# Performance work log

Hardware: AMD Instinct MI355X
Metric: run time of the kernel (lower is better)

## Reference

```python
import jax, jax.numpy as jnp
import numpy as np

B, N, D, H, K, FFN = 8, 256, 512, 16, 4, 2048
DK = D // H
NEG = -1e12


def _lin(k, i, o):
    return jax.random.normal(k, (i, o), jnp.float32) / np.sqrt(i)


def setup_inputs() -> dict:
    key = jax.random.key(0)
    ks = jax.random.split(key, 12)
    return {
        "x": jax.random.normal(ks[0], (B, N, D), jnp.float32),
        "dist": jax.random.uniform(ks[1], (B, N - 1, N - 1), jnp.float32) * 10.0,
        "dist_bar": jnp.array([1.5, 3.0, 5.0, 8.0], jnp.float32),
        "attn_bias": 0.1 * jax.random.normal(ks[2], (B, K, N, N), jnp.float32),
        "mask": jnp.ones((B, 1, N, N), jnp.int32),
        "num_heads": H,
        "Wq": _lin(ks[3], D, D), "bq": jnp.zeros((D,), jnp.float32),
        "Wk": _lin(ks[4], D, D), "bk": jnp.zeros((D,), jnp.float32),
        "Wv": _lin(ks[5], D, D), "bv": jnp.zeros((D,), jnp.float32),
        "W1": _lin(ks[6], K * D, D), "b1": jnp.zeros((D,), jnp.float32),
        "W2": _lin(ks[7], D, D), "b2": jnp.zeros((D,), jnp.float32),
        "g1": jnp.ones((D,), jnp.float32), "be1": jnp.zeros((D,), jnp.float32),
        "Wf1": _lin(ks[8], D, FFN), "bf1": jnp.zeros((FFN,), jnp.float32),
        "Wf2": _lin(ks[9], FFN, D), "bf2": jnp.zeros((D,), jnp.float32),
        "g2": jnp.ones((D,), jnp.float32), "be2": jnp.zeros((D,), jnp.float32),
    }


def _ln(x, g, b, eps=1e-6):
    m = jnp.mean(x, -1, keepdims=True)
    v = jnp.mean((x - m) ** 2, -1, keepdims=True)
    return (x - m) / jnp.sqrt(v + eps) * g + b


def _forward(x, dist, dist_bar, attn_bias, mask, num_heads,
             Wq, bq, Wk, bk, Wv, bv, W1, b1, W2, b2, g1, be1,
             Wf1, bf1, Wf2, bf2, g2, be2):
    Bn, Nn, Dn = x.shape
    Hh = num_heads
    dk = Dn // Hh
    Kk = dist_bar.shape[0]

    q = (x @ Wq + bq).reshape(Bn, Nn, Hh, dk).transpose(0, 2, 1, 3)  # [B,H,N,dk]
    k = (x @ Wk + bk).reshape(Bn, Nn, Hh, dk).transpose(0, 2, 1, 3)
    v = (x @ Wv + bv).reshape(Bn, Nn, Hh, dk).transpose(0, 2, 1, 3)

    scores = jnp.einsum('bhnd,bhmd->bhnm', q, k) / np.sqrt(dk)      # [B,H,N,N]
    # expand over scales and add bias: [B,H,K,N,N]
    scores = scores[:, :, None, :, :] + attn_bias[:, None, :, :, :]
    # padding mask [B,1,N,N] -> broadcast over H,K
    scores = jnp.where(mask[:, None] == 0, NEG, scores)

    # build padded distance with super node (row/col 0 distance = 0)
    nd = jnp.ones((Bn, Nn, Nn), x.dtype)
    nd = nd.at[:, 1:, 1:].set(dist)
    nd = nd.at[:, 0, :].set(0.0).at[:, :, 0].set(0.0)
    masks = nd[:, None, None, :, :] < dist_bar.reshape(1, 1, Kk, 1, 1)  # [B,1,K,N,N]
    masks = masks.at[:, :, :, 0, :].set(True).at[:, :, :, :, 0].set(True)

    scores = jnp.where(masks, scores, NEG)
    attn = jax.nn.softmax(scores, axis=-1)                           # [B,H,K,N,N]

    msg = jnp.einsum('bhknm,bhmd->bhknd', attn, v)                   # [B,H,K,N,dk]
    # faithful to torch: transpose(1,2).view(B,H*K,N,dk) then transpose(2,3).view(B,N,-1)
    msg = jnp.transpose(msg, (0, 2, 1, 3, 4)).reshape(Bn, Kk * Hh, Nn, dk)
    msg = jnp.transpose(msg, (0, 1, 3, 2)).reshape(Bn, Nn, Kk * Hh * dk)

    h = jax.nn.silu(msg @ W1 + b1) @ W2 + b2
    y = _ln(h + x, g1, be1)

    f = jax.nn.gelu(y @ Wf1 + bf1, approximate=False) @ Wf2 + bf2
    out = _ln(f + y, g2, be2)
    return out


def reference(x, dist, dist_bar, attn_bias, mask, num_heads,
              Wq, bq, Wk, bk, Wv, bv, W1, b1, W2, b2, g1, be1,
              Wf1, bf1, Wf2, bf2, g2, be2):
    return _forward(x, dist, dist_bar, attn_bias, mask, num_heads,
                    Wq, bq, Wk, bk, Wv, bv, W1, b1, W2, b2, g1, be1,
                    Wf1, bf1, Wf2, bf2, g2, be2)
```

## Files before the change

kernel.cpp:

```cpp
#include <hip/hip_runtime.h>
#include <math.h>

#define BB 8
#define NN 256
#define DD 512
#define HH 16
#define KK 4
#define DKK 32
#define FFN_ 2048
#define NEGV -1e12f

typedef __attribute__((ext_vector_type(8))) short bf16x8;
typedef __attribute__((ext_vector_type(4))) float f32x4;

__device__ __forceinline__ unsigned short f2bf(float f) {
    union { float f; unsigned int u; } v; v.f = f;
    unsigned int r = (v.u + 0x7FFFu + ((v.u >> 16) & 1u)) >> 16;
    return (unsigned short)r;
}
__device__ __forceinline__ float bf2f(unsigned short u) {
    union { unsigned int i; float f; } v; v.i = ((unsigned int)u) << 16;
    return v.f;
}
__device__ __forceinline__ void gload_lds16(const unsigned short* g, unsigned short* l) {
    __builtin_amdgcn_global_load_lds(
        (const __attribute__((address_space(1))) void*)g,
        (__attribute__((address_space(3))) void*)l, 16, 0, 0);
}

__global__ __launch_bounds__(256) void prep_kernel(
    const float* __restrict__ x,
    const float* __restrict__ Wq, const float* __restrict__ Wk,
    const float* __restrict__ Wv, const float* __restrict__ W1,
    const float* __restrict__ W2, const float* __restrict__ Wf1,
    const float* __restrict__ Wf2,
    const float* __restrict__ bq, const float* __restrict__ bk,
    const float* __restrict__ bv,
    unsigned short* __restrict__ xb, unsigned short* __restrict__ Wqkvt,
    unsigned short* __restrict__ W1t, unsigned short* __restrict__ W2t,
    unsigned short* __restrict__ Wf1t, unsigned short* __restrict__ Wf2t,
    float* __restrict__ bqkv)
{
    const int z = blockIdx.z;
    const int t = threadIdx.x;

    if (z == 7) {
        const int i0 = blockIdx.x * 1024 + t * 4;
        float4 xv = *(const float4*)(x + i0);
        ushort4 o;
        o.x = f2bf(xv.x); o.y = f2bf(xv.y); o.z = f2bf(xv.z); o.w = f2bf(xv.w);
        *(ushort4*)(xb + i0) = o;
        return;
    }
    if (z == 8) {
        if (blockIdx.x >= 6) return;
        const int i = blockIdx.x * 256 + t;
        float v = (i < 512) ? bq[i] : (i < 1024) ? bk[i - 512] : bv[i - 1024];
        bqkv[i] = v;
        return;
    }

    const float* src; unsigned short* dst; int Kd, Nd;
    switch (z) {
        case 0: src = Wq;  dst = Wqkvt;              Kd = 512;  Nd = 512;  break;
        case 1: src = Wk;  dst = Wqkvt + 512 * 512;  Kd = 512;  Nd = 512;  break;
        case 2: src = Wv;  dst = Wqkvt + 1024 * 512; Kd = 512;  Nd = 512;  break;
        case 3: src = W1;  dst = W1t;  Kd = 2048; Nd = 512;  break;
        case 4: src = W2;  dst = W2t;  Kd = 512;  Nd = 512;  break;
        case 5: src = Wf1; dst = Wf1t; Kd = 512;  Nd = 2048; break;
        default: src = Wf2; dst = Wf2t; Kd = 2048; Nd = 512; break;
    }
    const int ktiles = Kd / 32, ntiles = Nd / 32;
    const int ti = blockIdx.x;
    if (ti >= ktiles * ntiles) return;
    const int k0 = (ti % ktiles) * 32, n0 = (ti / ktiles) * 32;

    __shared__ float tile[32][33];
    const int xx = t & 31, yy = t >> 5;
    #pragma unroll
    for (int r = 0; r < 4; ++r)
        tile[yy * 4 + r][xx] = src[(size_t)(k0 + yy * 4 + r) * Nd + n0 + xx];
    __syncthreads();
    #pragma unroll
    for (int r = 0; r < 4; ++r)
        dst[(size_t)(n0 + yy * 4 + r) * Kd + k0 + xx] = f2bf(tile[xx][yy * 4 + r]);
}

__global__ __launch_bounds__(256) void prep_bias(
    const float* __restrict__ attn_bias, const int* __restrict__ mask,
    const float* __restrict__ dist, const float* __restrict__ dist_bar,
    unsigned short* __restrict__ biasMs)
{
    const int bx = blockIdx.x;
    const int rg = bx & 63, ks = (bx >> 6) & 3, b = bx >> 8;
    const int m = threadIdx.x;
    const float bar = dist_bar[ks];

    ushort4 o;
    unsigned short* po = (unsigned short*)&o;
    #pragma unroll
    for (int i = 0; i < 4; ++i) {
        const int n = rg * 4 + i;
        const int mk = mask[((size_t)(b * NN) + n) * NN + m];
        bool allowed = (n == 0) || (m == 0);
        if (!allowed)
            allowed = dist[((size_t)(b * 255) + (n - 1)) * 255 + (m - 1)] < bar;
        const float bias = attn_bias[(((size_t)(b * KK) + ks) * NN + n) * NN + m];
        po[i] = f2bf((mk != 0 && allowed) ? bias : NEGV);
    }
    *(ushort4*)(biasMs + (size_t)bx * 1024 + m * 4) = o;
}

template<int ACT, int EPI>
__global__ __launch_bounds__(256) void mfma_gemm128(
    const unsigned short* __restrict__ A, const unsigned short* __restrict__ Bt,
    const float* __restrict__ bias, unsigned short* __restrict__ Cb,
    unsigned short* __restrict__ vT, int M, int N, int Kdim)
{
    __shared__ unsigned short As[128 * 64];
    __shared__ unsigned short Bs[128 * 64];

    const int t = threadIdx.x, lane = t & 63, wv = t >> 6;
    const int n0 = blockIdx.x * 128, m0 = blockIdx.y * 128;
    const int wm = wv >> 1, wn = wv & 1;
    const int L = lane & 15, qd = lane >> 4;
    const int sr = lane >> 3, sc = lane & 7;

    f32x4 acc[4][4];
    #pragma unroll
    for (int i = 0; i < 4; ++i)
        #pragma unroll
        for (int j = 0; j < 4; ++j) acc[i][j] = (f32x4){0.f, 0.f, 0.f, 0.f};

    for (int kt = 0; kt < Kdim; kt += 64) {
        #pragma unroll
        for (int p = 0; p < 4; ++p) {
            const int rbase = wv * 32 + p * 8;
            gload_lds16(A  + (size_t)(m0 + rbase + sr) * Kdim + kt + sc * 8,
                        As + rbase * 64);
            gload_lds16(Bt + (size_t)(n0 + rbase + sr) * Kdim + kt + sc * 8,
                        Bs + rbase * 64);
        }
        __syncthreads();
        #pragma unroll
        for (int s = 0; s < 2; ++s) {
            bf16x8 af[4], bf[4];
            #pragma unroll
            for (int i = 0; i < 4; ++i)
                af[i] = *(const bf16x8*)(As + (wm * 64 + i * 16 + L) * 64 + s * 32 + qd * 8);
            #pragma unroll
            for (int j = 0; j < 4; ++j)
                bf[j] = *(const bf16x8*)(Bs + (wn * 64 + j * 16 + L) * 64 + s * 32 + qd * 8);
            #pragma unroll
            for (int i = 0; i < 4; ++i)
                #pragma unroll
                for (int j = 0; j < 4; ++j)
                    acc[i][j] = __builtin_amdgcn_mfma_f32_16x16x32_bf16(af[i], bf[j], acc[i][j], 0, 0, 0);
        }
        __syncthreads();
    }

    #pragma unroll
    for (int j = 0; j < 4; ++j) {
        const int col = n0 + wn * 64 + j * 16 + L;
        const float bv = bias[col];
        #pragma unroll
        for (int i = 0; i < 4; ++i) {
            const int rowb = m0 + wm * 64 + i * 16 + qd * 4;
            if (EPI == 1 && col >= 1024) {
                ushort4 pk;
                unsigned short* pp = (unsigned short*)&pk;
                #pragma unroll
                for (int r = 0; r < 4; ++r) pp[r] = f2bf(acc[i][j][r] + bv);
                *(ushort4*)(vT + (size_t)(col - 1024) * 2048 + rowb) = pk;
            } else {
                #pragma unroll
                for (int r = 0; r < 4; ++r) {
                    float v = acc[i][j][r] + bv;
                    if (ACT == 1) v = v / (1.0f + __expf(-v));
                    else if (ACT == 2) v = 0.5f * v * (1.0f + erff(v * 0.70710678118654752f));
                    Cb[(size_t)(rowb + r) * N + col] = f2bf(v);
                }
            }
        }
    }
}

template<int ACT>
__global__ __launch_bounds__(256) void mfma_gemm64(
    const unsigned short* __restrict__ A, const unsigned short* __restrict__ Bt,
    const float* __restrict__ bias, unsigned short* __restrict__ Cb,
    int M, int N, int Kdim)
{
    __shared__ unsigned short As[64 * 64];
    __shared__ unsigned short Bs[64 * 64];

    const int t = threadIdx.x, lane = t & 63, wv = t >> 6;
    const int n0 = blockIdx.x * 64, m0 = blockIdx.y * 64;
    const int r8 = lane >> 3, c8 = lane & 7;
    const int L = lane & 15, qd = lane >> 4;

    f32x4 acc[4];
    #pragma unroll
    for (int j = 0; j < 4; ++j) acc[j] = (f32x4){0.f, 0.f, 0.f, 0.f};

    for (int kt = 0; kt < Kdim; kt += 64) {
        #pragma unroll
        for (int i = 0; i < 2; ++i) {
            const int rbase = wv * 16 + i * 8;
            gload_lds16(A  + (size_t)(m0 + rbase + r8) * Kdim + kt + c8 * 8, As + rbase * 64);
            gload_lds16(Bt + (size_t)(n0 + rbase + r8) * Kdim + kt + c8 * 8, Bs + rbase * 64);
        }
        __syncthreads();
        #pragma unroll
        for (int s = 0; s < 2; ++s) {
            const bf16x8 a = *(const bf16x8*)(As + (wv * 16 + L) * 64 + s * 32 + qd * 8);
            #pragma unroll
            for (int j = 0; j < 4; ++j) {
                const bf16x8 b = *(const bf16x8*)(Bs + (j * 16 + L) * 64 + s * 32 + qd * 8);
                acc[j] = __builtin_amdgcn_mfma_f32_16x16x32_bf16(a, b, acc[j], 0, 0, 0);
            }
        }
        __syncthreads();
    }

    #pragma unroll
    for (int j = 0; j < 4; ++j) {
        const int col = n0 + j * 16 + L;
        const float bv = bias[col];
        #pragma unroll
        for (int r = 0; r < 4; ++r) {
            const int row = m0 + wv * 16 + qd * 4 + r;
            float v = acc[j][r] + bv;
            if (ACT == 1) v = v / (1.0f + __expf(-v));
            else if (ACT == 2) v = 0.5f * v * (1.0f + erff(v * 0.70710678118654752f));
            Cb[(size_t)row * N + col] = f2bf(v);
        }
    }
}

__global__ __launch_bounds__(256) void attn_kernel(
    const unsigned short* __restrict__ qkvb, const unsigned short* __restrict__ vT,
    const unsigned short* __restrict__ biasMs, unsigned short* __restrict__ msgT)
{
    const int qt = blockIdx.x, h = blockIdx.y, b = blockIdx.z;
    const int q0 = qt * 64;
    const int t = threadIdx.x, lane = t & 63, wv = t >> 6;
    const int L = lane & 15, qd = lane >> 4;

    __shared__ unsigned short Qs[64 * 32];
    __shared__ unsigned short Ks[256 * 32];
    __shared__ unsigned short Vs[32 * 264];
    __shared__ unsigned short Ps[64 * 264];
    __shared__ unsigned short Ot[32 * 72];

    {
        const int r = lane >> 2, c = lane & 3;
        gload_lds16(qkvb + (size_t)(b * NN + q0 + wv * 16 + r) * 1536 + h * DKK + c * 8,
                    Qs + wv * 16 * 32);
        #pragma unroll
        for (int p = 0; p < 4; ++p)
            gload_lds16(qkvb + (size_t)(b * NN + p * 64 + wv * 16 + r) * 1536 + 512 + h * DKK + c * 8,
                        Ks + (p * 64 + wv * 16) * 32);
    }
    {
        const int vr = t >> 3, seg = t & 7;
        const unsigned short* gv = vT + (size_t)(h * DKK + vr) * 2048 + b * NN + seg * 32;
        #pragma unroll
        for (int i = 0; i < 4; ++i) {
            bf16x8 vv = *(const bf16x8*)(gv + i * 8);
            *(bf16x8*)(Vs + vr * 264 + seg * 32 + i * 8) = vv;
        }
    }
    __syncthreads();

    f32x4 S[16];
    #pragma unroll
    for (int j = 0; j < 16; ++j) S[j] = (f32x4){0.f, 0.f, 0.f, 0.f};
    {
        const bf16x8 aq = *(const bf16x8*)(Qs + (wv * 16 + L) * 32 + qd * 8);
        #pragma unroll
        for (int j = 0; j < 16; ++j) {
            const bf16x8 bk = *(const bf16x8*)(Ks + (j * 16 + L) * 32 + qd * 8);
            S[j] = __builtin_amdgcn_mfma_f32_16x16x32_bf16(aq, bk, S[j], 0, 0, 0);
        }
    }
    const float scale = 0.17677669529663687f;
    const int rgb = (q0 + wv * 16) >> 2;

    for (int ks = 0; ks < KK; ++ks) {
        const unsigned short* bp = biasMs + ((size_t)((b * KK + ks) * 64 + rgb + qd)) * 1024;

        ushort4 b4[16];
        float mx[4] = {-3e38f, -3e38f, -3e38f, -3e38f};
        #pragma unroll
        for (int j = 0; j < 16; ++j) {
            b4[j] = *(const ushort4*)(bp + (j * 16 + L) * 4);
            const unsigned short* pb = (const unsigned short*)&b4[j];
            #pragma unroll
            for (int r = 0; r < 4; ++r)
                mx[r] = fmaxf(mx[r], S[j][r] * scale + bf2f(pb[r]));
        }
        #pragma unroll
        for (int off = 8; off > 0; off >>= 1)
            #pragma unroll
            for (int r = 0; r < 4; ++r)
                mx[r] = fmaxf(mx[r], __shfl_xor(mx[r], off));

        float sm[4] = {0.f, 0.f, 0.f, 0.f};
        #pragma unroll
        for (int j = 0; j < 16; ++j) {
            const unsigned short* pb = (const unsigned short*)&b4[j];
            #pragma unroll
            for (int r = 0; r < 4; ++r) {
                const float e = __expf(S[j][r] * scale + bf2f(pb[r]) - mx[r]);
                sm[r] += e;
                Ps[(wv * 16 + qd * 4 + r) * 264 + j * 16 + L] = f2bf(e);
            }
        }
        #pragma unroll
        for (int off = 8; off > 0; off >>= 1)
            #pragma unroll
            for (int r = 0; r < 4; ++r)
                sm[r] += __shfl_xor(sm[r], off);
        float inv[4];
        #pragma unroll
        for (int r = 0; r < 4; ++r) inv[r] = 1.0f / sm[r];

        f32x4 O[2];
        O[0] = (f32x4){0.f, 0.f, 0.f, 0.f};
        O[1] = (f32x4){0.f, 0.f, 0.f, 0.f};
        #pragma unroll
        for (int kc = 0; kc < 8; ++kc) {
            const bf16x8 ap = *(const bf16x8*)(Ps + (wv * 16 + L) * 264 + kc * 32 + qd * 8);
            #pragma unroll
            for (int jt = 0; jt < 2; ++jt) {
                const bf16x8 bv = *(const bf16x8*)(Vs + (jt * 16 + L) * 264 + kc * 32 + qd * 8);
                O[jt] = __builtin_amdgcn_mfma_f32_16x16x32_bf16(ap, bv, O[jt], 0, 0, 0);
            }
        }
        #pragma unroll
        for (int jt = 0; jt < 2; ++jt)
            #pragma unroll
            for (int r = 0; r < 4; ++r)
                Ot[(jt * 16 + L) * 72 + wv * 16 + qd * 4 + r] = f2bf(O[jt][r] * inv[r]);
        __syncthreads();

        {
            const int dd = t >> 3, cc = t & 7;
            bf16x8 ov = *(const bf16x8*)(Ot + dd * 72 + cc * 8);
            *(bf16x8*)(msgT + (size_t)b * 524288 +
                       ((size_t)((ks * HH + h) * DKK + dd)) * NN + q0 + cc * 8) = ov;
        }
        __syncthreads();
    }
}

__global__ __launch_bounds__(256) void ln_kernel(
    const unsigned short* __restrict__ a, const float* __restrict__ r,
    const float* __restrict__ g, const float* __restrict__ be,
    float* __restrict__ out, unsigned short* __restrict__ outb)
{
    const int row = blockIdx.x;
    const int t = threadIdx.x;
    __shared__ float red[256];

    const size_t base = (size_t)row * DD;
    const float z0 = bf2f(a[base + t]) + r[base + t];
    const float z1 = bf2f(a[base + 256 + t]) + r[base + 256 + t];

    red[t] = z0 + z1; __syncthreads();
    for (int s = 128; s > 0; s >>= 1) {
        if (t < s) red[t] += red[t + s];
        __syncthreads();
    }
    const float mean = red[0] * (1.0f / 512.0f); __syncthreads();

    const float d0 = z0 - mean, d1 = z1 - mean;
    red[t] = d0 * d0 + d1 * d1; __syncthreads();
    for (int s = 128; s > 0; s >>= 1) {
        if (t < s) red[t] += red[t + s];
        __syncthreads();
    }
    const float inv = rsqrtf(red[0] * (1.0f / 512.0f) + 1e-6f);

    const float o0 = d0 * inv * g[t] + be[t];
    const float o1 = d1 * inv * g[256 + t] + be[256 + t];
    out[base + t] = o0;
    out[base + 256 + t] = o1;
    if (outb) {
        outb[base + t] = f2bf(o0);
        outb[base + 256 + t] = f2bf(o1);
    }
}

extern "C" void kernel_launch(void* const* d_in, const int* in_sizes, int n_in,
                              void* d_out, int out_size, void* d_ws, size_t ws_size,
                              hipStream_t stream)
{
    const float* x         = (const float*)d_in[0];
    const float* dist      = (const float*)d_in[1];
    const float* dist_bar  = (const float*)d_in[2];
    const float* attn_bias = (const float*)d_in[3];
    const int*   mask      = (const int*)d_in[4];
    const float* Wq  = (const float*)d_in[6];  const float* bq  = (const float*)d_in[7];
    const float* Wk  = (const float*)d_in[8];  const float* bk  = (const float*)d_in[9];
    const float* Wv  = (const float*)d_in[10]; const float* bv  = (const float*)d_in[11];
    const float* W1  = (const float*)d_in[12]; const float* b1  = (const float*)d_in[13];
    const float* W2  = (const float*)d_in[14]; const float* b2  = (const float*)d_in[15];
    const float* g1  = (const float*)d_in[16]; const float* be1 = (const float*)d_in[17];
    const float* Wf1 = (const float*)d_in[18]; const float* bf1 = (const float*)d_in[19];
    const float* Wf2 = (const float*)d_in[20]; const float* bf2 = (const float*)d_in[21];
    const float* g2  = (const float*)d_in[22]; const float* be2 = (const float*)d_in[23];

    float* ws = (float*)d_ws;
    unsigned short* qkvb   = (unsigned short*)(ws + 0);
    float*          yb     = ws + 0;
    unsigned short* vT     = (unsigned short*)(ws + 1572864);
    unsigned short* h1     = (unsigned short*)(ws + 1572864);
    unsigned short* xb     = (unsigned short*)(ws + 2097152);
    unsigned short* msgT   = (unsigned short*)(ws + 2097152);
    unsigned short* g3     = msgT;
    unsigned short* biasMs = (unsigned short*)(ws + 4194304);
    unsigned short* h2     = (unsigned short*)(ws + 4194304);
    unsigned short* fb     = h2;
    float*          bqkv   = ws + 5242880;
    unsigned short* yb16   = (unsigned short*)(ws + 5242880);
    unsigned short* Wqkvt  = (unsigned short*)(ws + 5767168);
    unsigned short* W1t    = (unsigned short*)(ws + 6160384);
    unsigned short* W2t    = (unsigned short*)(ws + 6684672);
    unsigned short* Wf1t   = (unsigned short*)(ws + 6815744);
    unsigned short* Wf2t   = (unsigned short*)(ws + 7340032);
    float*          outp   = (float*)d_out;

    dim3 thr(256);
    const int M = BB * NN;

    prep_kernel<<<dim3(1024, 1, 9), thr, 0, stream>>>(
        x, Wq, Wk, Wv, W1, W2, Wf1, Wf2, bq, bk, bv,
        xb, Wqkvt, W1t, W2t, Wf1t, Wf2t, bqkv);
    prep_bias<<<dim3(2048), thr, 0, stream>>>(attn_bias, mask, dist, dist_bar, biasMs);

    mfma_gemm128<0,1><<<dim3(12, 16), thr, 0, stream>>>(xb, Wqkvt, bqkv, qkvb, vT, M, 1536, DD);

    attn_kernel<<<dim3(4, HH, BB), thr, 0, stream>>>(qkvb, vT, biasMs, msgT);

    mfma_gemm64<1><<<dim3(8, 32), thr, 0, stream>>>(msgT, W1t, b1, h1, M, DD, 2048);
    mfma_gemm64<0><<<dim3(8, 32), thr, 0, stream>>>(h1, W2t, b2, h2, M, DD, DD);

    ln_kernel<<<dim3(M), thr, 0, stream>>>(h2, x, g1, be1, yb, yb16);

    mfma_gemm128<2,0><<<dim3(16, 16), thr, 0, stream>>>(yb16, Wf1t, bf1, g3, nullptr, M, FFN_, DD);
    mfma_gemm64<0><<<dim3(8, 32), thr, 0, stream>>>(g3, Wf2t, bf2, fb, M, DD, 2048);

    ln_kernel<<<dim3(M), thr, 0, stream>>>(fb, yb, g2, be2, outp, nullptr);
}
```

Baseline: 267.0 us.

## Use 512-thread 128x128 GEMMs with split-K partials and fused bias/LN finishers

Replaces the 128x128 and 64x64 GEMM kernels with one 512-thread, 8-wave 128x128 tile kernel. The narrow-N GEMMs (W1, W2, Wf2) use split-K into fp32 partial buffers, reduced by new finisher kernels that also apply bias plus SiLU, or bias, residual and LayerNorm. The bias/mask preparation is merged into the weight-prep kernel as an extra grid slice, which removes a launch, and the workspace layout is rearranged to hold the partials. The aim is more waves per CU and better GPU fill for the 2048x512 outputs. The cost is extra fp32 partial traffic and additional finisher passes.

```diff
diff --git a/kernel.cpp b/kernel.cpp
--- a/kernel.cpp
+++ b/kernel.cpp
@@ -36,15 +36,18 @@
     const float* __restrict__ Wf2,
     const float* __restrict__ bq, const float* __restrict__ bk,
     const float* __restrict__ bv,
+    const float* __restrict__ attn_bias, const int* __restrict__ mask,
+    const float* __restrict__ dist, const float* __restrict__ dist_bar,
     unsigned short* __restrict__ xb, unsigned short* __restrict__ Wqkvt,
     unsigned short* __restrict__ W1t, unsigned short* __restrict__ W2t,
     unsigned short* __restrict__ Wf1t, unsigned short* __restrict__ Wf2t,
-    float* __restrict__ bqkv)
+    float* __restrict__ bqkv, unsigned short* __restrict__ biasMs)
 {
     const int z = blockIdx.z;
     const int t = threadIdx.x;
 
     if (z == 7) {
+        if (blockIdx.x >= 1024) return;
         const int i0 = blockIdx.x * 1024 + t * 4;
         float4 xv = *(const float4*)(x + i0);
         ushort4 o;
@@ -57,6 +60,26 @@
         const int i = blockIdx.x * 256 + t;
         float v = (i < 512) ? bq[i] : (i < 1024) ? bk[i - 512] : bv[i - 1024];
         bqkv[i] = v;
+        return;
+    }
+    if (z == 9) {
+        const int bx = blockIdx.x;
+        const int rg = bx & 63, ks = (bx >> 6) & 3, b = bx >> 8;
+        const int m = t;
+        const float bar = dist_bar[ks];
+        ushort4 o;
+        unsigned short* po = (unsigned short*)&o;
+        #pragma unroll
+        for (int i = 0; i < 4; ++i) {
+            const int n = rg * 4 + i;
+            const int mk = mask[((size_t)(b * NN) + n) * NN + m];
+            bool allowed = (n == 0) || (m == 0);
+            if (!allowed)
+                allowed = dist[((size_t)(b * 255) + (n - 1)) * 255 + (m - 1)] < bar;
+            const float bias = attn_bias[(((size_t)(b * KK) + ks) * NN + n) * NN + m];
+            po[i] = f2bf((mk != 0 && allowed) ? bias : NEGV);
+        }
+        *(ushort4*)(biasMs + (size_t)bx * 1024 + m * 4) = o;
         return;
     }
 
@@ -86,36 +109,12 @@
         dst[(size_t)(n0 + yy * 4 + r) * Kd + k0 + xx] = f2bf(tile[xx][yy * 4 + r]);
 }
 
-__global__ __launch_bounds__(256) void prep_bias(
-    const float* __restrict__ attn_bias, const int* __restrict__ mask,
-    const float* __restrict__ dist, const float* __restrict__ dist_bar,
-    unsigned short* __restrict__ biasMs)
-{
-    const int bx = blockIdx.x;
-    const int rg = bx & 63, ks = (bx >> 6) & 3, b = bx >> 8;
-    const int m = threadIdx.x;
-    const float bar = dist_bar[ks];
-
-    ushort4 o;
-    unsigned short* po = (unsigned short*)&o;
-    #pragma unroll
-    for (int i = 0; i < 4; ++i) {
-        const int n = rg * 4 + i;
-        const int mk = mask[((size_t)(b * NN) + n) * NN + m];
-        bool allowed = (n == 0) || (m == 0);
-        if (!allowed)
-            allowed = dist[((size_t)(b * 255) + (n - 1)) * 255 + (m - 1)] < bar;
-        const float bias = attn_bias[(((size_t)(b * KK) + ks) * NN + n) * NN + m];
-        po[i] = f2bf((mk != 0 && allowed) ? bias : NEGV);
-    }
-    *(ushort4*)(biasMs + (size_t)bx * 1024 + m * 4) = o;
-}
-
-template<int ACT, int EPI>
-__global__ __launch_bounds__(256) void mfma_gemm128(
+template<int ACT, int EPI, int KSPLIT>
+__global__ __launch_bounds__(512) void mfma_gemm512(
     const unsigned short* __restrict__ A, const unsigned short* __restrict__ Bt,
     const float* __restrict__ bias, unsigned short* __restrict__ Cb,
-    unsigned short* __restrict__ vT, int M, int N, int Kdim)
+    unsigned short* __restrict__ vT, float* __restrict__ Cp,
+    int M, int N, int Kdim)
 {
     __shared__ unsigned short As[128 * 64];
     __shared__ unsigned short Bs[128 * 64];
@@ -126,16 +125,19 @@
     const int L = lane & 15, qd = lane >> 4;
     const int sr = lane >> 3, sc = lane & 7;
 
-    f32x4 acc[4][4];
-    #pragma unroll
-    for (int i = 0; i < 4; ++i)
+    const int ksub = Kdim / KSPLIT;
+    const int kbeg = blockIdx.z * ksub;
+
+    f32x4 acc[2][4];
+    #pragma unroll
+    for (int i = 0; i < 2; ++i)
         #pragma unroll
         for (int j = 0; j < 4; ++j) acc[i][j] = (f32x4){0.f, 0.f, 0.f, 0.f};
 
-    for (int kt = 0; kt < Kdim; kt += 64) {
-        #pragma unroll
-        for (int p = 0; p < 4; ++p) {
-            const int rbase = wv * 32 + p * 8;
+    for (int kt = kbeg; kt < kbeg + ksub; kt += 64) {
+        #pragma unroll
+        for (int p = 0; p < 2; ++p) {
+            const int rbase = wv * 16 + p * 8;
             gload_lds16(A  + (size_t)(m0 + rbase + sr) * Kdim + kt + sc * 8,
                         As + rbase * 64);
             gload_lds16(Bt + (size_t)(n0 + rbase + sr) * Kdim + kt + sc * 8,
@@ -144,18 +146,18 @@
         __syncthreads();
         #pragma unroll
         for (int s = 0; s < 2; ++s) {
-            bf16x8 af[4], bf[4];
-            #pragma unroll
-            for (int i = 0; i < 4; ++i)
-                af[i] = *(const bf16x8*)(As + (wm * 64 + i * 16 + L) * 64 + s * 32 + qd * 8);
+            bf16x8 af[2], bfb[4];
+            #pragma unroll
+            for (int i = 0; i < 2; ++i)
+                af[i] = *(const bf16x8*)(As + (wm * 32 + i * 16 + L) * 64 + s * 32 + qd * 8);
             #pragma unroll
             for (int j = 0; j < 4; ++j)
-                bf[j] = *(const bf16x8*)(Bs + (wn * 64 + j * 16 + L) * 64 + s * 32 + qd * 8);
-            #pragma unroll
-            for (int i = 0; i < 4; ++i)
+                bfb[j] = *(const bf16x8*)(Bs + (wn * 64 + j * 16 + L) * 64 + s * 32 + qd * 8);
+            #pragma unroll
+            for (int i = 0; i < 2; ++i)
                 #pragma unroll
                 for (int j = 0; j < 4; ++j)
-                    acc[i][j] = __builtin_amdgcn_mfma_f32_16x16x32_bf16(af[i], bf[j], acc[i][j], 0, 0, 0);
+                    acc[i][j] = __builtin_amdgcn_mfma_f32_16x16x32_bf16(af[i], bfb[j], acc[i][j], 0, 0, 0);
         }
         __syncthreads();
     }
@@ -163,17 +165,22 @@
     #pragma unroll
     for (int j = 0; j < 4; ++j) {
         const int col = n0 + wn * 64 + j * 16 + L;
-        const float bv = bias[col];
-        #pragma unroll
-        for (int i = 0; i < 4; ++i) {
-            const int rowb = m0 + wm * 64 + i * 16 + qd * 4;
-            if (EPI == 1 && col >= 1024) {
+        #pragma unroll
+        for (int i = 0; i < 2; ++i) {
+            const int rowb = m0 + wm * 32 + i * 16 + qd * 4;
+            if (EPI == 2) {
+                float* cp = Cp + (size_t)blockIdx.z * M * N + (size_t)rowb * N + col;
+                #pragma unroll
+                for (int r = 0; r < 4; ++r) cp[(size_t)r * N] = acc[i][j][r];
+            } else if (EPI == 1 && col >= 1024) {
+                const float bv = bias[col];
                 ushort4 pk;
                 unsigned short* pp = (unsigned short*)&pk;
                 #pragma unroll
                 for (int r = 0; r < 4; ++r) pp[r] = f2bf(acc[i][j][r] + bv);
                 *(ushort4*)(vT + (size_t)(col - 1024) * 2048 + rowb) = pk;
             } else {
+                const float bv = bias[col];
                 #pragma unroll
                 for (int r = 0; r < 4; ++r) {
                     float v = acc[i][j][r] + bv;
@@ -186,56 +193,70 @@
     }
 }
 
-template<int ACT>
-__global__ __launch_bounds__(256) void mfma_gemm64(
-    const unsigned short* __restrict__ A, const unsigned short* __restrict__ Bt,
-    const float* __restrict__ bias, unsigned short* __restrict__ Cb,
-    int M, int N, int Kdim)
-{
-    __shared__ unsigned short As[64 * 64];
-    __shared__ unsigned short Bs[64 * 64];
-
-    const int t = threadIdx.x, lane = t & 63, wv = t >> 6;
-    const int n0 = blockIdx.x * 64, m0 = blockIdx.y * 64;
-    const int r8 = lane >> 3, c8 = lane & 7;
-    const int L = lane & 15, qd = lane >> 4;
-
-    f32x4 acc[4];
-    #pragma unroll
-    for (int j = 0; j < 4; ++j) acc[j] = (f32x4){0.f, 0.f, 0.f, 0.f};
-
-    for (int kt = 0; kt < Kdim; kt += 64) {
-        #pragma unroll
-        for (int i = 0; i < 2; ++i) {
-            const int rbase = wv * 16 + i * 8;
-            gload_lds16(A  + (size_t)(m0 + rbase + r8) * Kdim + kt + c8 * 8, As + rbase * 64);
-            gload_lds16(Bt + (size_t)(n0 + rbase + r8) * Kdim + kt + c8 * 8, Bs + rbase * 64);
-        }
-        __syncthreads();
-        #pragma unroll
-        for (int s = 0; s < 2; ++s) {
-            const bf16x8 a = *(const bf16x8*)(As + (wv * 16 + L) * 64 + s * 32 + qd * 8);
-            #pragma unroll
-            for (int j = 0; j < 4; ++j) {
-                const bf16x8 b = *(const bf16x8*)(Bs + (j * 16 + L) * 64 + s * 32 + qd * 8);
-                acc[j] = __builtin_amdgcn_mfma_f32_16x16x32_bf16(a, b, acc[j], 0, 0, 0);
-            }
-        }
-        __syncthreads();
-    }
-
-    #pragma unroll
-    for (int j = 0; j < 4; ++j) {
-        const int col = n0 + j * 16 + L;
-        const float bv = bias[col];
-        #pragma unroll
-        for (int r = 0; r < 4; ++r) {
-            const int row = m0 + wv * 16 + qd * 4 + r;
-            float v = acc[j][r] + bv;
-            if (ACT == 1) v = v / (1.0f + __expf(-v));
-            else if (ACT == 2) v = 0.5f * v * (1.0f + erff(v * 0.70710678118654752f));
-            Cb[(size_t)row * N + col] = f2bf(v);
-        }
+__global__ __launch_bounds__(256) void fin_silu(
+    const float* __restrict__ Cp, const float* __restrict__ bias,
+    unsigned short* __restrict__ out)
+{
+    const int row = blockIdx.x, t = threadIdx.x;
+    const int c0 = t * 2;
+    const size_t base = (size_t)row * DD;
+    float sx = 0.f, sy = 0.f;
+    #pragma unroll
+    for (int z = 0; z < 4; ++z) {
+        const float2 p = *(const float2*)(Cp + (size_t)z * (2048u * 512u) + base + c0);
+        sx += p.x; sy += p.y;
+    }
+    float v0 = sx + bias[c0], v1 = sy + bias[c0 + 1];
+    v0 = v0 / (1.0f + __expf(-v0));
+    v1 = v1 / (1.0f + __expf(-v1));
+    ushort2 pk; pk.x = f2bf(v0); pk.y = f2bf(v1);
+    *(ushort2*)(out + base + c0) = pk;
+}
+
+template<int KS, int OUT16>
+__global__ __launch_bounds__(256) void fin_ln(
+    const float* __restrict__ Cp, const float* __restrict__ bias,
+    const float* __restrict__ res, const float* __restrict__ g,
+    const float* __restrict__ be, float* __restrict__ out,
+    unsigned short* __restrict__ outb)
+{
+    const int row = blockIdx.x, t = threadIdx.x;
+    const int c0 = t * 2;
+    const size_t base = (size_t)row * DD;
+    __shared__ float red[256];
+
+    float sx = 0.f, sy = 0.f;
+    #pragma unroll
+    for (int z = 0; z < KS; ++z) {
+        const float2 p = *(const float2*)(Cp + (size_t)z * (2048u * 512u) + base + c0);
+        sx += p.x; sy += p.y;
+    }
+    const float2 rv = *(const float2*)(res + base + c0);
+    const float z0 = sx + bias[c0]     + rv.x;
+    const float z1 = sy + bias[c0 + 1] + rv.y;
+
+    red[t] = z0 + z1; __syncthreads();
+    for (int s = 128; s > 0; s >>= 1) {
+        if (t < s) red[t] += red[t + s];
+        __syncthreads();
+    }
+    const float mean = red[0] * (1.0f / 512.0f); __syncthreads();
+
+    const float d0 = z0 - mean, d1 = z1 - mean;
+    red[t] = d0 * d0 + d1 * d1; __syncthreads();
+    for (int s = 128; s > 0; s >>= 1) {
+        if (t < s) red[t] += red[t + s];
+        __syncthreads();
+    }
+    const float inv = rsqrtf(red[0] * (1.0f / 512.0f) + 1e-6f);
+
+    const float o0 = d0 * inv * g[c0]     + be[c0];
+    const float o1 = d1 * inv * g[c0 + 1] + be[c0 + 1];
+    out[base + c0]     = o0;
+    out[base + c0 + 1] = o1;
+    if (OUT16) {
+        ushort2 pk; pk.x = f2bf(o0); pk.y = f2bf(o1);
+        *(ushort2*)(outb + base + c0) = pk;
     }
 }
 
@@ -353,44 +374,6 @@
                        ((size_t)((ks * HH + h) * DKK + dd)) * NN + q0 + cc * 8) = ov;
         }
         __syncthreads();
-    }
-}
-
-__global__ __launch_bounds__(256) void ln_kernel(
-    const unsigned short* __restrict__ a, const float* __restrict__ r,
-    const float* __restrict__ g, const float* __restrict__ be,
-    float* __restrict__ out, unsigned short* __restrict__ outb)
-{
-    const int row = blockIdx.x;
-    const int t = threadIdx.x;
-    __shared__ float red[256];
-
-    const size_t base = (size_t)row * DD;
-    const float z0 = bf2f(a[base + t]) + r[base + t];
-    const float z1 = bf2f(a[base + 256 + t]) + r[base + 256 + t];
-
-    red[t] = z0 + z1; __syncthreads();
-    for (int s = 128; s > 0; s >>= 1) {
-        if (t < s) red[t] += red[t + s];
-        __syncthreads();
-    }
-    const float mean = red[0] * (1.0f / 512.0f); __syncthreads();
-
-    const float d0 = z0 - mean, d1 = z1 - mean;
-    red[t] = d0 * d0 + d1 * d1; __syncthreads();
-    for (int s = 128; s > 0; s >>= 1) {
-        if (t < s) red[t] += red[t + s];
-        __syncthreads();
-    }
-    const float inv = rsqrtf(red[0] * (1.0f / 512.0f) + 1e-6f);
-
-    const float o0 = d0 * inv * g[t] + be[t];
-    const float o1 = d1 * inv * g[256 + t] + be[256 + t];
-    out[base + t] = o0;
-    out[base + 256 + t] = o1;
-    if (outb) {
-        outb[base + t] = f2bf(o0);
-        outb[base + 256 + t] = f2bf(o1);
     }
 }
 
@@ -415,43 +398,47 @@
 
     float* ws = (float*)d_ws;
     unsigned short* qkvb   = (unsigned short*)(ws + 0);
-    float*          yb     = ws + 0;
     unsigned short* vT     = (unsigned short*)(ws + 1572864);
-    unsigned short* h1     = (unsigned short*)(ws + 1572864);
     unsigned short* xb     = (unsigned short*)(ws + 2097152);
-    unsigned short* msgT   = (unsigned short*)(ws + 2097152);
+    unsigned short* msgT   = (unsigned short*)(ws + 2621440);
     unsigned short* g3     = msgT;
-    unsigned short* biasMs = (unsigned short*)(ws + 4194304);
-    unsigned short* h2     = (unsigned short*)(ws + 4194304);
-    unsigned short* fb     = h2;
-    float*          bqkv   = ws + 5242880;
-    unsigned short* yb16   = (unsigned short*)(ws + 5242880);
-    unsigned short* Wqkvt  = (unsigned short*)(ws + 5767168);
-    unsigned short* W1t    = (unsigned short*)(ws + 6160384);
-    unsigned short* W2t    = (unsigned short*)(ws + 6684672);
-    unsigned short* Wf1t   = (unsigned short*)(ws + 6815744);
-    unsigned short* Wf2t   = (unsigned short*)(ws + 7340032);
+    unsigned short* biasMs = (unsigned short*)(ws + 4718592);
+    float*          bqkv   = ws + 5767168;
+    unsigned short* h1     = (unsigned short*)(ws + 5771264);
+    float*          yb     = ws + 6295552;
+    unsigned short* yb16   = (unsigned short*)(ws + 7344128);
+    unsigned short* Wqkvt  = (unsigned short*)(ws + 7868416);
+    unsigned short* W1t    = (unsigned short*)(ws + 8261632);
+    unsigned short* W2t    = (unsigned short*)(ws + 8785920);
+    unsigned short* Wf1t   = (unsigned short*)(ws + 8916992);
+    unsigned short* Wf2t   = (unsigned short*)(ws + 9441280);
+    float*          part   = ws + 9965568;
     float*          outp   = (float*)d_out;
 
-    dim3 thr(256);
     const int M = BB * NN;
 
-    prep_kernel<<<dim3(1024, 1, 9), thr, 0, stream>>>(
+    prep_kernel<<<dim3(2048, 1, 10), dim3(256), 0, stream>>>(
         x, Wq, Wk, Wv, W1, W2, Wf1, Wf2, bq, bk, bv,
-        xb, Wqkvt, W1t, W2t, Wf1t, Wf2t, bqkv);
-    prep_bias<<<dim3(2048), thr, 0, stream>>>(attn_bias, mask, dist, dist_bar, biasMs);
-
-    mfma_gemm128<0,1><<<dim3(12, 16), thr, 0, stream>>>(xb, Wqkvt, bqkv, qkvb, vT, M, 1536, DD);
-
-    attn_kernel<<<dim3(4, HH, BB), thr, 0, stream>>>(qkvb, vT, biasMs, msgT);
-
-    mfma_gemm64<1><<<dim3(8, 32), thr, 0, stream>>>(msgT, W1t, b1, h1, M, DD, 2048);
-    mfma_gemm64<0><<<dim3(8, 32), thr, 0, stream>>>(h1, W2t, b2, h2, M, DD, DD);
-
-    ln_kernel<<<dim3(M), thr, 0, stream>>>(h2, x, g1, be1, yb, yb16);
-
-    mfma_gemm128<2,0><<<dim3(16, 16), thr, 0, stream>>>(yb16, Wf1t, bf1, g3, nullptr, M, FFN_, DD);
-    mfma_gemm64<0><<<dim3(8, 32), thr, 0, stream>>>(g3, Wf2t, bf2, fb, M, DD, 2048);
-
-    ln_kernel<<<dim3(M), thr, 0, stream>>>(fb, yb, g2, be2, outp, nullptr);
-}
+        attn_bias, mask, dist, dist_bar,
+        xb, Wqkvt, W1t, W2t, Wf1t, Wf2t, bqkv, biasMs);
+
+    mfma_gemm512<0,1,1><<<dim3(12, 16, 1), dim3(512), 0, stream>>>(
+        xb, Wqkvt, bqkv, qkvb, vT, nullptr, M, 1536, DD);
+
+    attn_kernel<<<dim3(4, HH, BB), dim3(256), 0, stream>>>(qkvb, vT, biasMs, msgT);
+
+    mfma_gemm512<0,2,4><<<dim3(4, 16, 4), dim3(512), 0, stream>>>(
+        msgT, W1t, nullptr, nullptr, nullptr, part, M, DD, 2048);
+    fin_silu<<<dim3(M), dim3(256), 0, stream>>>(part, b1, h1);
+
+    mfma_gemm512<0,2,2><<<dim3(4, 16, 2), dim3(512), 0, stream>>>(
+        h1, W2t, nullptr, nullptr, nullptr, part, M, DD, DD);
+    fin_ln<2,1><<<dim3(M), dim3(256), 0, stream>>>(part, b2, x, g1, be1, yb, yb16);
+
+    mfma_gemm512<2,0,1><<<dim3(16, 16, 1), dim3(512), 0, stream>>>(
+        yb16, Wf1t, bf1, g3, nullptr, nullptr, M, FFN_, DD);
+
+    mfma_gemm512<0,2,4><<<dim3(4, 16, 4), dim3(512), 0, stream>>>(
+        g3, Wf2t, nullptr, nullptr, nullptr, part, M, DD, 2048);
+    fin_ln<4,0><<<dim3(M), dim3(256), 0, stream>>>(part, bf2, yb, g2, be2, outp, nullptr);
+}
```

New measurement: 254.0 us. -4.9%, faster.

## Fuse output GEMMs with LayerNorm, fold bias prep, widen 128-tile GEMM to 512 threads

Applied to the files above, without the earlier changes.

The W2 and Wf2 projections are fused with the residual add and LayerNorm in a new gemm_ln kernel. Each of its blocks computes 16 full 512-wide rows, so the bf16 intermediate round trip and the separate LN launches go away. The attention bias/mask preparation is merged into prep_kernel as an extra grid slice. The 128x128 GEMM now runs with 8 waves of 512 threads, each computing a 32x64 sub-tile, to raise occupancy. The trade-off is that gemm_ln launches only 128 blocks, and every block reloads the whole 512-column weight slab each K step, which lowers parallelism for the K=2048 FFN down-projection.

```diff
diff --git a/kernel.cpp b/kernel.cpp
--- a/kernel.cpp
+++ b/kernel.cpp
@@ -36,15 +36,18 @@
     const float* __restrict__ Wf2,
     const float* __restrict__ bq, const float* __restrict__ bk,
     const float* __restrict__ bv,
+    const float* __restrict__ attn_bias, const int* __restrict__ mask,
+    const float* __restrict__ dist, const float* __restrict__ dist_bar,
     unsigned short* __restrict__ xb, unsigned short* __restrict__ Wqkvt,
     unsigned short* __restrict__ W1t, unsigned short* __restrict__ W2t,
     unsigned short* __restrict__ Wf1t, unsigned short* __restrict__ Wf2t,
-    float* __restrict__ bqkv)
+    float* __restrict__ bqkv, unsigned short* __restrict__ biasMs)
 {
     const int z = blockIdx.z;
     const int t = threadIdx.x;
 
     if (z == 7) {
+        if (blockIdx.x >= 1024) return;
         const int i0 = blockIdx.x * 1024 + t * 4;
         float4 xv = *(const float4*)(x + i0);
         ushort4 o;
@@ -57,6 +60,25 @@
         const int i = blockIdx.x * 256 + t;
         float v = (i < 512) ? bq[i] : (i < 1024) ? bk[i - 512] : bv[i - 1024];
         bqkv[i] = v;
+        return;
+    }
+    if (z == 9) {
+        const int bx = blockIdx.x;
+        const int rg = bx & 63, ks = (bx >> 6) & 3, b = bx >> 8;
+        const int m = t;
+        const float bar = dist_bar[ks];
+        ushort4 o; unsigned short* po = (unsigned short*)&o;
+        #pragma unroll
+        for (int i = 0; i < 4; ++i) {
+            const int n = rg * 4 + i;
+            const int mk = mask[((size_t)(b * NN) + n) * NN + m];
+            bool allowed = (n == 0) || (m == 0);
+            if (!allowed)
+                allowed = dist[((size_t)(b * 255) + (n - 1)) * 255 + (m - 1)] < bar;
+            const float bias = attn_bias[(((size_t)(b * KK) + ks) * NN + n) * NN + m];
+            po[i] = f2bf((mk != 0 && allowed) ? bias : NEGV);
+        }
+        *(ushort4*)(biasMs + (size_t)bx * 1024 + m * 4) = o;
         return;
     }
 
@@ -86,33 +108,8 @@
         dst[(size_t)(n0 + yy * 4 + r) * Kd + k0 + xx] = f2bf(tile[xx][yy * 4 + r]);
 }
 
-__global__ __launch_bounds__(256) void prep_bias(
-    const float* __restrict__ attn_bias, const int* __restrict__ mask,
-    const float* __restrict__ dist, const float* __restrict__ dist_bar,
-    unsigned short* __restrict__ biasMs)
-{
-    const int bx = blockIdx.x;
-    const int rg = bx & 63, ks = (bx >> 6) & 3, b = bx >> 8;
-    const int m = threadIdx.x;
-    const float bar = dist_bar[ks];
-
-    ushort4 o;
-    unsigned short* po = (unsigned short*)&o;
-    #pragma unroll
-    for (int i = 0; i < 4; ++i) {
-        const int n = rg * 4 + i;
-        const int mk = mask[((size_t)(b * NN) + n) * NN + m];
-        bool allowed = (n == 0) || (m == 0);
-        if (!allowed)
-            allowed = dist[((size_t)(b * 255) + (n - 1)) * 255 + (m - 1)] < bar;
-        const float bias = attn_bias[(((size_t)(b * KK) + ks) * NN + n) * NN + m];
-        po[i] = f2bf((mk != 0 && allowed) ? bias : NEGV);
-    }
-    *(ushort4*)(biasMs + (size_t)bx * 1024 + m * 4) = o;
-}
-
 template<int ACT, int EPI>
-__global__ __launch_bounds__(256) void mfma_gemm128(
+__global__ __launch_bounds__(512) void mfma_gemm512(
     const unsigned short* __restrict__ A, const unsigned short* __restrict__ Bt,
     const float* __restrict__ bias, unsigned short* __restrict__ Cb,
     unsigned short* __restrict__ vT, int M, int N, int Kdim)
@@ -126,16 +123,16 @@
     const int L = lane & 15, qd = lane >> 4;
     const int sr = lane >> 3, sc = lane & 7;
 
-    f32x4 acc[4][4];
-    #pragma unroll
-    for (int i = 0; i < 4; ++i)
+    f32x4 acc[2][4];
+    #pragma unroll
+    for (int i = 0; i < 2; ++i)
         #pragma unroll
         for (int j = 0; j < 4; ++j) acc[i][j] = (f32x4){0.f, 0.f, 0.f, 0.f};
 
     for (int kt = 0; kt < Kdim; kt += 64) {
         #pragma unroll
-        for (int p = 0; p < 4; ++p) {
-            const int rbase = wv * 32 + p * 8;
+        for (int p = 0; p < 2; ++p) {
+            const int rbase = wv * 16 + p * 8;
             gload_lds16(A  + (size_t)(m0 + rbase + sr) * Kdim + kt + sc * 8,
                         As + rbase * 64);
             gload_lds16(Bt + (size_t)(n0 + rbase + sr) * Kdim + kt + sc * 8,
@@ -144,18 +141,18 @@
         __syncthreads();
         #pragma unroll
         for (int s = 0; s < 2; ++s) {
-            bf16x8 af[4], bf[4];
-            #pragma unroll
-            for (int i = 0; i < 4; ++i)
-                af[i] = *(const bf16x8*)(As + (wm * 64 + i * 16 + L) * 64 + s * 32 + qd * 8);
+            bf16x8 af[2], bfb[4];
+            #pragma unroll
+            for (int i = 0; i < 2; ++i)
+                af[i] = *(const bf16x8*)(As + (wm * 32 + i * 16 + L) * 64 + s * 32 + qd * 8);
             #pragma unroll
             for (int j = 0; j < 4; ++j)
-                bf[j] = *(const bf16x8*)(Bs + (wn * 64 + j * 16 + L) * 64 + s * 32 + qd * 8);
-            #pragma unroll
-            for (int i = 0; i < 4; ++i)
+                bfb[j] = *(const bf16x8*)(Bs + (wn * 64 + j * 16 + L) * 64 + s * 32 + qd * 8);
+            #pragma unroll
+            for (int i = 0; i < 2; ++i)
                 #pragma unroll
                 for (int j = 0; j < 4; ++j)
-                    acc[i][j] = __builtin_amdgcn_mfma_f32_16x16x32_bf16(af[i], bf[j], acc[i][j], 0, 0, 0);
+                    acc[i][j] = __builtin_amdgcn_mfma_f32_16x16x32_bf16(af[i], bfb[j], acc[i][j], 0, 0, 0);
         }
         __syncthreads();
     }
@@ -165,11 +162,10 @@
         const int col = n0 + wn * 64 + j * 16 + L;
         const float bv = bias[col];
         #pragma unroll
-        for (int i = 0; i < 4; ++i) {
-            const int rowb = m0 + wm * 64 + i * 16 + qd * 4;
+        for (int i = 0; i < 2; ++i) {
+            const int rowb = m0 + wm * 32 + i * 16 + qd * 4;
             if (EPI == 1 && col >= 1024) {
-                ushort4 pk;
-                unsigned short* pp = (unsigned short*)&pk;
+                ushort4 pk; unsigned short* pp = (unsigned short*)&pk;
                 #pragma unroll
                 for (int r = 0; r < 4; ++r) pp[r] = f2bf(acc[i][j][r] + bv);
                 *(ushort4*)(vT + (size_t)(col - 1024) * 2048 + rowb) = pk;
@@ -177,8 +173,7 @@
                 #pragma unroll
                 for (int r = 0; r < 4; ++r) {
                     float v = acc[i][j][r] + bv;
-                    if (ACT == 1) v = v / (1.0f + __expf(-v));
-                    else if (ACT == 2) v = 0.5f * v * (1.0f + erff(v * 0.70710678118654752f));
+                    if (ACT == 2) v = 0.5f * v * (1.0f + erff(v * 0.70710678118654752f));
                     Cb[(size_t)(rowb + r) * N + col] = f2bf(v);
                 }
             }
@@ -233,8 +228,121 @@
             const int row = m0 + wv * 16 + qd * 4 + r;
             float v = acc[j][r] + bv;
             if (ACT == 1) v = v / (1.0f + __expf(-v));
-            else if (ACT == 2) v = 0.5f * v * (1.0f + erff(v * 0.70710678118654752f));
             Cb[(size_t)row * N + col] = f2bf(v);
+        }
+    }
+}
+
+template<int KD, int OUT16>
+__global__ __launch_bounds__(256) void gemm_ln(
+    const unsigned short* __restrict__ A, const unsigned short* __restrict__ Bt,
+    const float* __restrict__ bias, const float* __restrict__ res,
+    const float* __restrict__ g, const float* __restrict__ be,
+    float* __restrict__ out, unsigned short* __restrict__ outb)
+{
+    __shared__ unsigned short As[16 * 64];
+    __shared__ unsigned short Bs[512 * 64];
+    __shared__ float red1[4][16];
+    __shared__ float red2[4][16];
+
+    const int t = threadIdx.x, lane = t & 63, wv = t >> 6;
+    const int L = lane & 15, qd = lane >> 4;
+    const int m0 = blockIdx.x * 16;
+
+    f32x4 acc[8];
+    #pragma unroll
+    for (int j = 0; j < 8; ++j) acc[j] = (f32x4){0.f, 0.f, 0.f, 0.f};
+
+    for (int kt = 0; kt < KD; kt += 64) {
+        if (t < 128)
+            gload_lds16(A + (size_t)(m0 + (t >> 3)) * KD + kt + (t & 7) * 8,
+                        As + (t >> 3) * 64);
+        #pragma unroll
+        for (int i = 0; i < 16; ++i)
+            gload_lds16(Bt + (size_t)(i * 32 + (t >> 3)) * KD + kt + (t & 7) * 8,
+                        Bs + (i * 32 + (t >> 3)) * 64);
+        __syncthreads();
+        #pragma unroll
+        for (int s = 0; s < 2; ++s) {
+            const bf16x8 a = *(const bf16x8*)(As + L * 64 + s * 32 + qd * 8);
+            #pragma unroll
+            for (int j = 0; j < 8; ++j) {
+                const bf16x8 b = *(const bf16x8*)(Bs + (wv * 128 + j * 16 + L) * 64 + s * 32 + qd * 8);
+                acc[j] = __builtin_amdgcn_mfma_f32_16x16x32_bf16(a, b, acc[j], 0, 0, 0);
+            }
+        }
+        __syncthreads();
+    }
+
+    float val[8][4];
+    #pragma unroll
+    for (int j = 0; j < 8; ++j) {
+        const int col = wv * 128 + j * 16 + L;
+        const float bv = bias[col];
+        #pragma unroll
+        for (int r = 0; r < 4; ++r) {
+            const int row = m0 + qd * 4 + r;
+            val[j][r] = acc[j][r] + bv + res[(size_t)row * DD + col];
+        }
+    }
+
+    float s[4] = {0.f, 0.f, 0.f, 0.f};
+    #pragma unroll
+    for (int j = 0; j < 8; ++j)
+        #pragma unroll
+        for (int r = 0; r < 4; ++r) s[r] += val[j][r];
+    #pragma unroll
+    for (int off = 8; off > 0; off >>= 1)
+        #pragma unroll
+        for (int r = 0; r < 4; ++r) s[r] += __shfl_xor(s[r], off);
+    if (L == 0) {
+        #pragma unroll
+        for (int r = 0; r < 4; ++r) red1[wv][qd * 4 + r] = s[r];
+    }
+    __syncthreads();
+    float mean[4];
+    #pragma unroll
+    for (int r = 0; r < 4; ++r) {
+        const int rr = qd * 4 + r;
+        mean[r] = (red1[0][rr] + red1[1][rr] + red1[2][rr] + red1[3][rr]) * (1.0f / 512.0f);
+    }
+
+    float v2[4] = {0.f, 0.f, 0.f, 0.f};
+    #pragma unroll
+    for (int j = 0; j < 8; ++j)
+        #pragma unroll
+        for (int r = 0; r < 4; ++r) {
+            const float d = val[j][r] - mean[r];
+            val[j][r] = d;
+            v2[r] += d * d;
+        }
+    #pragma unroll
+    for (int off = 8; off > 0; off >>= 1)
+        #pragma unroll
+        for (int r = 0; r < 4; ++r) v2[r] += __shfl_xor(v2[r], off);
+    if (L == 0) {
+        #pragma unroll
+        for (int r = 0; r < 4; ++r) red2[wv][qd * 4 + r] = v2[r];
+    }
+    __syncthreads();
+    float inv[4];
+    #pragma unroll
+    for (int r = 0; r < 4; ++r) {
+        const int rr = qd * 4 + r;
+        const float var = (red2[0][rr] + red2[1][rr] + red2[2][rr] + red2[3][rr]) * (1.0f / 512.0f);
+        inv[r] = rsqrtf(var + 1e-6f);
+    }
+
+    #pragma unroll
+    for (int j = 0; j < 8; ++j) {
+        const int col = wv * 128 + j * 16 + L;
+        const float gc = g[col], bc = be[col];
+        #pragma unroll
+        for (int r = 0; r < 4; ++r) {
+            const int row = m0 + qd * 4 + r;
+            const float o = val[j][r] * inv[r] * gc + bc;
+            out[(size_t)row * DD + col] = o;
+            if (OUT16) outb[(size_t)row * DD + col] = f2bf(o);
         }
     }
 }
@@ -304,8 +412,7 @@
         #pragma unroll
         for (int off = 8; off > 0; off >>= 1)
             #pragma unroll
-            for (int r = 0; r < 4; ++r)
-                mx[r] = fmaxf(mx[r], __shfl_xor(mx[r], off));
+            for (int r = 0; r < 4; ++r) mx[r] = fmaxf(mx[r], __shfl_xor(mx[r], off));
 
         float sm[4] = {0.f, 0.f, 0.f, 0.f};
         #pragma unroll
@@ -321,8 +428,7 @@
         #pragma unroll
         for (int off = 8; off > 0; off >>= 1)
             #pragma unroll
-            for (int r = 0; r < 4; ++r)
-                sm[r] += __shfl_xor(sm[r], off);
+            for (int r = 0; r < 4; ++r) sm[r] += __shfl_xor(sm[r], off);
         float inv[4];
         #pragma unroll
         for (int r = 0; r < 4; ++r) inv[r] = 1.0f / sm[r];
@@ -353,44 +459,6 @@
                        ((size_t)((ks * HH + h) * DKK + dd)) * NN + q0 + cc * 8) = ov;
         }
         __syncthreads();
-    }
-}
-
-__global__ __launch_bounds__(256) void ln_kernel(
-    const unsigned short* __restrict__ a, const float* __restrict__ r,
-    const float* __restrict__ g, const float* __restrict__ be,
-    float* __restrict__ out, unsigned short* __restrict__ outb)
-{
-    const int row = blockIdx.x;
-    const int t = threadIdx.x;
-    __shared__ float red[256];
-
-    const size_t base = (size_t)row * DD;
-    const float z0 = bf2f(a[base + t]) + r[base + t];
-    const float z1 = bf2f(a[base + 256 + t]) + r[base + 256 + t];
-
-    red[t] = z0 + z1; __syncthreads();
-    for (int s = 128; s > 0; s >>= 1) {
-        if (t < s) red[t] += red[t + s];
-        __syncthreads();
-    }
-    const float mean = red[0] * (1.0f / 512.0f); __syncthreads();
-
-    const float d0 = z0 - mean, d1 = z1 - mean;
-    red[t] = d0 * d0 + d1 * d1; __syncthreads();
-    for (int s = 128; s > 0; s >>= 1) {
-        if (t < s) red[t] += red[t + s];
-        __syncthreads();
-    }
-    const float inv = rsqrtf(red[0] * (1.0f / 512.0f) + 1e-6f);
-
-    const float o0 = d0 * inv * g[t] + be[t];
-    const float o1 = d1 * inv * g[256 + t] + be[256 + t];
-    out[base + t] = o0;
-    out[base + 256 + t] = o1;
-    if (outb) {
-        outb[base + t] = f2bf(o0);
-        outb[base + 256 + t] = f2bf(o1);
     }
 }
 
@@ -415,43 +483,42 @@
 
     float* ws = (float*)d_ws;
     unsigned short* qkvb   = (unsigned short*)(ws + 0);
-    float*          yb     = ws + 0;
     unsigned short* vT     = (unsigned short*)(ws + 1572864);
-    unsigned short* h1     = (unsigned short*)(ws + 1572864);
     unsigned short* xb     = (unsigned short*)(ws + 2097152);
-    unsigned short* msgT   = (unsigned short*)(ws + 2097152);
+    unsigned short* msgT   = (unsigned short*)(ws + 2621440);
     unsigned short* g3     = msgT;
-    unsigned short* biasMs = (unsigned short*)(ws + 4194304);
-    unsigned short* h2     = (unsigned short*)(ws + 4194304);
-    unsigned short* fb     = h2;
-    float*          bqkv   = ws + 5242880;
-    unsigned short* yb16   = (unsigned short*)(ws + 5242880);
-    unsigned short* Wqkvt  = (unsigned short*)(ws + 5767168);
-    unsigned short* W1t    = (unsigned short*)(ws + 6160384);
-    unsigned short* W2t    = (unsigned short*)(ws + 6684672);
-    unsigned short* Wf1t   = (unsigned short*)(ws + 6815744);
-    unsigned short* Wf2t   = (unsigned short*)(ws + 7340032);
+    unsigned short* biasMs = (unsigned short*)(ws + 4718592);
+    float*          bqkv   = ws + 5767168;
+    unsigned short* h1     = (unsigned short*)(ws + 5771264);
+    float*          yb     = ws + 6295552;
+    unsigned short* yb16   = (unsigned short*)(ws + 7344128);
+    unsigned short* Wqkvt  = (unsigned short*)(ws + 7868416);
+    unsigned short* W1t    = (unsigned short*)(ws + 8261632);
+    unsigned short* W2t    = (unsigned short*)(ws + 8785920);
+    unsigned short* Wf1t   = (unsigned short*)(ws + 8916992);
+    unsigned short* Wf2t   = (unsigned short*)(ws + 9441280);
     float*          outp   = (float*)d_out;
 
-    dim3 thr(256);
     const int M = BB * NN;
 
-    prep_kernel<<<dim3(1024, 1, 9), thr, 0, stream>>>(
+    prep_kernel<<<dim3(2048, 1, 10), dim3(256), 0, stream>>>(
         x, Wq, Wk, Wv, W1, W2, Wf1, Wf2, bq, bk, bv,
-        xb, Wqkvt, W1t, W2t, Wf1t, Wf2t, bqkv);
-    prep_bias<<<dim3(2048), thr, 0, stream>>>(attn_bias, mask, dist, dist_bar, biasMs);
-
-    mfma_gemm128<0,1><<<dim3(12, 16), thr, 0, stream>>>(xb, Wqkvt, bqkv, qkvb, vT, M, 1536, DD);
-
-    attn_kernel<<<dim3(4, HH, BB), thr, 0, stream>>>(qkvb, vT, biasMs, msgT);
-
-    mfma_gemm64<1><<<dim3(8, 32), thr, 0, stream>>>(msgT, W1t, b1, h1, M, DD, 2048);
-    mfma_gemm64<0><<<dim3(8, 32), thr, 0, stream>>>(h1, W2t, b2, h2, M, DD, DD);
-
-    ln_kernel<<<dim3(M), thr, 0, stream>>>(h2, x, g1, be1, yb, yb16);
-
-    mfma_gemm128<2,0><<<dim3(16, 16), thr, 0, stream>>>(yb16, Wf1t, bf1, g3, nullptr, M, FFN_, DD);
-    mfma_gemm64<0><<<dim3(8, 32), thr, 0, stream>>>(g3, Wf2t, bf2, fb, M, DD, 2048);
-
-    ln_kernel<<<dim3(M), thr, 0, stream>>>(fb, yb, g2, be2, outp, nullptr);
-}
+        attn_bias, mask, dist, dist_bar,
+        xb, Wqkvt, W1t, W2t, Wf1t, Wf2t, bqkv, biasMs);
+
+    mfma_gemm512<0, 1><<<dim3(12, 16), dim3(512), 0, stream>>>(
+        xb, Wqkvt, bqkv, qkvb, vT, M, 1536, DD);
+
+    attn_kernel<<<dim3(4, HH, BB), dim3(256), 0, stream>>>(qkvb, vT, biasMs, msgT);
+
+    mfma_gemm64<1><<<dim3(8, 32), dim3(256), 0, stream>>>(msgT, W1t, b1, h1, M, DD, 2048);
+
+    gemm_ln<512, 1><<<dim3(128), dim3(256), 0, stream>>>(
+        h1, W2t, b2, x, g1, be1, yb, yb16);
+
+    mfma_gemm512<2, 0><<<dim3(16, 16), dim3(512), 0, stream>>>(
+        yb16, Wf1t, bf1, g3, nullptr, M, FFN_, DD);
+
+    gemm_ln<2048, 0><<<dim3(128), dim3(256), 0, stream>>>(
+        g3, Wf2t, bf2, yb, g2, be2, outp, nullptr);
+}
```

After: 283.5 us. +6.2%, slower.
